# Kernel optimization log

Hardware: AMD Instinct MI355X
Metric: run time of the kernel (lower is better)

Reference implementation:

```python
import jax, jax.numpy as jnp
import numpy as np

N_NODES = 50000
N_EDGES = 800000
IN_DIM = 128
HID = 64
HEADS = 4
EDGE_DIM = 3
NEG_SLOPE = 0.2  # PyG GATv2 default


def setup_inputs() -> dict:
    key = jax.random.key(0)
    ks = jax.random.split(key, 16)
    def glorot(k, shape):
        fan_in = shape[0]
        return (jax.random.normal(k, shape, jnp.float32) / jnp.sqrt(jnp.float32(fan_in)))
    x = jax.random.normal(ks[0], (N_NODES, IN_DIM), jnp.float32)
    edge_attr = jax.random.normal(ks[1], (N_EDGES, EDGE_DIM), jnp.float32)
    edge_index = jax.random.randint(ks[2], (2, N_EDGES), 0, N_NODES, jnp.int32)
    # layer 1: GATv2Conv(IN_DIM -> HID, heads=HEADS, edge_dim=3, concat=True)
    W1l = glorot(ks[3], (IN_DIM, HEADS * HID))
    W1r = glorot(ks[4], (IN_DIM, HEADS * HID))
    W1e = glorot(ks[5], (EDGE_DIM, HEADS * HID))
    att1 = glorot(ks[6], (HEADS, HID))
    b1 = jnp.zeros((HEADS * HID,), jnp.float32)
    # layer 2: GATv2Conv(HEADS*HID -> 1, heads=1, edge_dim=3, concat=False)
    W2l = glorot(ks[7], (HEADS * HID, 1))
    W2r = glorot(ks[8], (HEADS * HID, 1))
    W2e = glorot(ks[9], (EDGE_DIM, 1))
    att2 = glorot(ks[10], (1, 1))
    b2 = jnp.zeros((1,), jnp.float32)
    return {"x": x, "edge_attr": edge_attr, "W1l": W1l, "W1r": W1r, "W1e": W1e,
            "att1": att1, "b1": b1, "W2l": W2l, "W2r": W2r, "W2e": W2e,
            "att2": att2, "b2": b2, "edge_index": edge_index}


def _add_self_loops(edge_index, edge_attr, n_nodes):
    # PyG GATv2Conv add_self_loops=True with fill_value='mean' for edge_attr
    loops = jnp.arange(n_nodes, dtype=edge_index.dtype)
    ei = jnp.concatenate([edge_index, jnp.stack([loops, loops])], axis=1)
    loop_attr = jnp.broadcast_to(edge_attr.mean(axis=0, keepdims=True),
                                 (n_nodes, edge_attr.shape[1]))
    ea = jnp.concatenate([edge_attr, loop_attr], axis=0)
    return ei, ea


def _gatv2(x, edge_index, edge_attr, Wl, Wr, We, att, bias, heads, concat):
    n = x.shape[0]
    c = Wl.shape[1] // heads
    src, dst = edge_index[0], edge_index[1]
    xl = (x @ Wl).reshape(n, heads, c)   # source-side transform
    xr = (x @ Wr).reshape(n, heads, c)   # target-side transform
    ef = (edge_attr @ We).reshape(-1, heads, c)
    m = jax.nn.leaky_relu(xl[src] + xr[dst] + ef, NEG_SLOPE)   # [E,H,C]
    logits = jnp.einsum('ehc,hc->eh', m, att)                  # [E,H]
    mx = jax.ops.segment_max(logits, dst, num_segments=n)      # segment softmax over dst
    a = jnp.exp(logits - mx[dst])
    denom = jax.ops.segment_sum(a, dst, num_segments=n)
    alpha = a / denom[dst]                                     # [E,H]
    out = jax.ops.segment_sum(xl[src] * alpha[:, :, None], dst, num_segments=n)  # [N,H,C]
    out = out.reshape(n, heads * c) if concat else out.mean(axis=1)
    return out + bias


def reference(x, edge_attr, W1l, W1r, W1e, att1, b1, W2l, W2r, W2e, att2, b2, edge_index):
    n = x.shape[0]
    ei, ea = _add_self_loops(edge_index, edge_attr, n)
    h = _gatv2(x, ei, ea, W1l, W1r, W1e, att1, b1, HEADS, True)
    h = jax.nn.elu(h)  # dropout identity in eval mode
    gat_scores = _gatv2(h, ei, ea, W2l, W2r, W2e, att2, b2, 1, False).squeeze(-1)
    portfolio_weights = jax.nn.softmax(gat_scores, axis=0)
    return portfolio_weights, gat_scores
```

## Files before the change

### kernel.cpp

```cpp
#include <hip/hip_runtime.h>
#include <hip/hip_bf16.h>
#include <hip/hip_fp16.h>

typedef __attribute__((ext_vector_type(8))) short short8;
typedef __attribute__((ext_vector_type(4))) float floatx4;
typedef __attribute__((ext_vector_type(4))) unsigned short ushortx4;
typedef _Float16 h2 __attribute__((ext_vector_type(2)));
typedef _Float16 h4 __attribute__((ext_vector_type(4)));
typedef _Float16 h8 __attribute__((ext_vector_type(8)));

#define N_NODESC 50000
#define MPAD     50016
#define N_EDGESC 800000
#define E_TOTC   850000
#define IN_DIMC  128
#define FDIM     256
#define HEADSC   4
#define HIDC     64
#define NEG_SLOPE 0.2f
#define RESCALE_THR 8.0f

#define SCAN_TILE 1024
#define SCAN_NB   ((N_NODESC + SCAN_TILE - 1) / SCAN_TILE)

__device__ __forceinline__ float wave_sum(float v){
  #pragma unroll
  for (int m = 32; m > 0; m >>= 1) v += __shfl_xor(v, m, 64);
  return v;
}
__device__ __forceinline__ float wave_max(float v){
  #pragma unroll
  for (int m = 32; m > 0; m >>= 1) v = fmaxf(v, __shfl_xor(v, m, 64));
  return v;
}

__device__ __forceinline__ h2 f2h2(float v){
  return __builtin_bit_cast(h2, __builtin_amdgcn_cvt_pkrtz(v, v));
}

__global__ __launch_bounds__(256) void k_mean(const float* __restrict__ ea,
                                              float* __restrict__ meanacc){
  float s0 = 0.f, s1 = 0.f, s2 = 0.f;
  for (int i = blockIdx.x * blockDim.x + threadIdx.x; i < N_EDGESC;
       i += gridDim.x * blockDim.x){
    s0 += ea[i*3+0]; s1 += ea[i*3+1]; s2 += ea[i*3+2];
  }
  s0 = wave_sum(s0); s1 = wave_sum(s1); s2 = wave_sum(s2);
  __shared__ float red[3][4];
  int lane = threadIdx.x & 63, w = threadIdx.x >> 6;
  if (lane == 0){ red[0][w] = s0; red[1][w] = s1; red[2][w] = s2; }
  __syncthreads();
  if (threadIdx.x == 0){
    float t0 = 0.f, t1 = 0.f, t2 = 0.f;
    for (int i = 0; i < 4; i++){ t0 += red[0][i]; t1 += red[1][i]; t2 += red[2][i]; }
    atomicAdd(&meanacc[0], t0); atomicAdd(&meanacc[1], t1); atomicAdd(&meanacc[2], t2);
  }
}

__global__ __launch_bounds__(256) void k_count(const int* __restrict__ ei,
                                               int* __restrict__ deg){
  int e = blockIdx.x * blockDim.x + threadIdx.x;
  if (e >= N_EDGESC) return;
  atomicAdd(&deg[ei[N_EDGESC + e]], 1);
}

__global__ __launch_bounds__(256) void k_cvtx(const float* __restrict__ x,
                                              _Float16* __restrict__ xb){
  size_t tid = (size_t)blockIdx.x * 256 + threadIdx.x;
  size_t base = tid * 4;
  const size_t NELEM = (size_t)N_NODESC * IN_DIMC;
  h4 o;
  if (base + 3 < NELEM){
    const float4* xp = (const float4*)(x + base);
    float4 v = *xp;
    o[0] = (_Float16)v.x; o[1] = (_Float16)v.y;
    o[2] = (_Float16)v.z; o[3] = (_Float16)v.w;
  } else {
    #pragma unroll
    for (int f = 0; f < 4; f++){
      size_t i = base + f;
      float v = (i < NELEM) ? x[i] : 0.f;
      o[f] = (_Float16)v;
    }
  }
  *(h4*)(xb + base) = o;
}

__global__ __launch_bounds__(256) void k_cvtw(const float* __restrict__ W1l,
                                              const float* __restrict__ W1r,
                                              _Float16* __restrict__ Bfrag){
  int idx = blockIdx.x * 256 + threadIdx.x;
  int mat = idx >> 15;
  int r   = idx & 32767;
  int k   = r >> 8, n = r & 255;
  float v = mat ? W1r[r] : W1l[r];
  int pos = (mat << 15) + (((k >> 3) << 8) + n) * 8 + (k & 7);
  Bfrag[pos] = (_Float16)v;
}

__global__ __launch_bounds__(256) void k_gemm_mfma(const _Float16* __restrict__ xb,
                                                   const _Float16* __restrict__ Bfrag,
                                                   _Float16* __restrict__ xl,
                                                   _Float16* __restrict__ xr){
  const int mat = blockIdx.y;
  const int r0  = blockIdx.x * 32;
  const int w = threadIdx.x >> 6, lane = threadIdx.x & 63;
  const int quad = lane >> 4, l16 = lane & 15;
  const _Float16* Bm = Bfrag + ((size_t)mat << 15);
  _Float16* C = mat ? xr : xl;

  h8 afr[2][4];
  #pragma unroll
  for (int ms = 0; ms < 2; ms++)
    #pragma unroll
    for (int ks = 0; ks < 4; ks++){
      const _Float16* p = xb + (size_t)(r0 + ms*16 + l16) * IN_DIMC + ks*32 + quad*8;
      afr[ms][ks] = *reinterpret_cast<const h8*>(p);
    }
  const int n0 = w * 64;
  floatx4 acc[2][4];
  #pragma unroll
  for (int ms = 0; ms < 2; ms++)
    #pragma unroll
    for (int ns = 0; ns < 4; ns++){
      floatx4 z = {0.f, 0.f, 0.f, 0.f};
      acc[ms][ns] = z;
    }
  #pragma unroll
  for (int ks = 0; ks < 4; ks++){
    #pragma unroll
    for (int ns = 0; ns < 4; ns++){
      int n = n0 + ns*16 + l16;
      int kblk = ks*4 + quad;
      h8 bfr = *reinterpret_cast<const h8*>(Bm + ((size_t)kblk*256 + n)*8);
      acc[0][ns] = __builtin_amdgcn_mfma_f32_16x16x32_f16(afr[0][ks], bfr, acc[0][ns], 0, 0, 0);
      acc[1][ns] = __builtin_amdgcn_mfma_f32_16x16x32_f16(afr[1][ks], bfr, acc[1][ns], 0, 0, 0);
    }
  }
  #pragma unroll
  for (int ms = 0; ms < 2; ms++)
    #pragma unroll
    for (int ns = 0; ns < 4; ns++){
      int col = n0 + ns*16 + l16;
      #pragma unroll
      for (int rg = 0; rg < 4; rg++){
        int row = r0 + ms*16 + quad*4 + rg;
        C[(size_t)row * FDIM + col] = (_Float16)acc[ms][ns][rg];
      }
    }
}

__global__ __launch_bounds__(256) void k_scan_pa(const int* __restrict__ deg,
                                                 int* __restrict__ pre,
                                                 int* __restrict__ bsum){
  int b = blockIdx.x, t = threadIdx.x;
  int lane = t & 63, w = t >> 6;
  int base = b * SCAN_TILE + t * 4;
  int4 v = {0, 0, 0, 0};
  if (base + 3 < N_NODESC){
    v = *(const int4*)(deg + base);
    v.x += 1; v.y += 1; v.z += 1; v.w += 1;
  } else {
    if (base + 0 < N_NODESC) v.x = deg[base + 0] + 1;
    if (base + 1 < N_NODESC) v.y = deg[base + 1] + 1;
    if (base + 2 < N_NODESC) v.z = deg[base + 2] + 1;
    if (base + 3 < N_NODESC) v.w = deg[base + 3] + 1;
  }
  int s = v.x + v.y + v.z + v.w;
  int inc = s;
  #pragma unroll
  for (int off = 1; off < 64; off <<= 1){
    int u = __shfl_up(inc, off, 64);
    if (lane >= off) inc += u;
  }
  __shared__ int wsum[4];
  if (lane == 63) wsum[w] = inc;
  __syncthreads();
  int wadd = 0;
  #pragma unroll
  for (int i = 0; i < 4; i++) if (i < w) wadd += wsum[i];
  int excl = inc - s + wadd;
  if (base + 3 < N_NODESC){
    int4 o;
    o.x = excl; o.y = o.x + v.x; o.z = o.y + v.y; o.w = o.z + v.z;
    *(int4*)(pre + base) = o;
  } else {
    int run = excl;
    if (base + 0 < N_NODESC){ pre[base + 0] = run; run += v.x; }
    if (base + 1 < N_NODESC){ pre[base + 1] = run; run += v.y; }
    if (base + 2 < N_NODESC){ pre[base + 2] = run; run += v.z; }
    if (base + 3 < N_NODESC){ pre[base + 3] = run; }
  }
  if (t == 255) bsum[b] = wsum[0] + wsum[1] + wsum[2] + wsum[3];
}

__global__ __launch_bounds__(64) void k_scan_pb(const int* __restrict__ bsum,
                                                int* __restrict__ boff,
                                                int* __restrict__ offsets){
  int lane = threadIdx.x;
  int s = (lane < SCAN_NB) ? bsum[lane] : 0;
  int inc = s;
  #pragma unroll
  for (int off = 1; off < 64; off <<= 1){
    int u = __shfl_up(inc, off, 64);
    if (lane >= off) inc += u;
  }
  if (lane < SCAN_NB) boff[lane] = inc - s;
  if (lane == 63) offsets[N_NODESC] = inc;
}

__global__ __launch_bounds__(256) void k_scan_pc(const int* __restrict__ pre,
                                                 const int* __restrict__ boff,
                                                 int* __restrict__ offsets,
                                                 int* __restrict__ cursor){
  int b = blockIdx.x;
  int base = b * SCAN_TILE + threadIdx.x * 4;
  int add = boff[b];
  if (base + 3 < N_NODESC){
    int4 p = *(const int4*)(pre + base);
    p.x += add; p.y += add; p.z += add; p.w += add;
    *(int4*)(offsets + base) = p;
    *(int4*)(cursor + base) = p;
  } else {
    #pragma unroll
    for (int f = 0; f < 4; f++){
      int i = base + f;
      if (i < N_NODESC){ int vv = pre[i] + add; offsets[i] = vv; cursor[i] = vv; }
    }
  }
}

__global__ __launch_bounds__(256) void k_scatter(const int* __restrict__ ei,
                                                 const float* __restrict__ ea,
                                                 const float* __restrict__ meanacc,
                                                 const int* __restrict__ offsets,
                                                 int* __restrict__ cursor,
                                                 float4* __restrict__ rec){
  int e = blockIdx.x * blockDim.x + threadIdx.x;
  if (e >= E_TOTC) return;
  int pos; float4 r;
  if (e < N_EDGESC){
    int src = ei[e], dst = ei[N_EDGESC + e];
    r.x = __int_as_float(src);
    r.y = ea[e*3+0]; r.z = ea[e*3+1]; r.w = ea[e*3+2];
    pos = atomicAdd(&cursor[dst], 1);
  } else {
    int i = e - N_EDGESC;
    const float inv = 1.0f / (float)N_EDGESC;
    r.x = __int_as_float(i);
    r.y = meanacc[0]*inv; r.z = meanacc[1]*inv; r.w = meanacc[2]*inv;
    pos = offsets[i + 1] - 1;
  }
  rec[pos] = r;
}

__global__ __launch_bounds__(256, 8) void k_attn1(const int* __restrict__ offsets,
                                                  const float4* __restrict__ rec,
                                                  const _Float16* __restrict__ xl,
                                                  const _Float16* __restrict__ xr,
                                                  const float* __restrict__ W1e,
                                                  const float* __restrict__ att1,
                                                  const float* __restrict__ b1,
                                                  const float* __restrict__ W2l,
                                                  const float* __restrict__ W2r,
                                                  float* __restrict__ sl,
                                                  float* __restrict__ sr){
  const int t = threadIdx.x, lane = t & 63, w = t >> 6;
  const int n = blockIdx.x * 4 + w;
  const int f0 = lane * 4;

  h2 xr01, xr23, w0a, w0b, w1a, w1b, w2a, w2b, at01, at23;
  {
    h4 xw = *(const h4*)(xr + (size_t)n * FDIM + f0);
    float4 a = *(const float4*)(W1e + f0);
    float4 b = *(const float4*)(W1e + FDIM + f0);
    float4 c = *(const float4*)(W1e + 2*FDIM + f0);
    float4 d = *(const float4*)(att1 + f0);
    xr01 = h2{xw[0], xw[1]};                  xr23 = h2{xw[2], xw[3]};
    w0a = h2{(_Float16)a.x, (_Float16)a.y};   w0b = h2{(_Float16)a.z, (_Float16)a.w};
    w1a = h2{(_Float16)b.x, (_Float16)b.y};   w1b = h2{(_Float16)b.z, (_Float16)b.w};
    w2a = h2{(_Float16)c.x, (_Float16)c.y};   w2b = h2{(_Float16)c.z, (_Float16)c.w};
    at01 = h2{(_Float16)d.x, (_Float16)d.y};  at23 = h2{(_Float16)d.z, (_Float16)d.w};
  }
  const h2 nsl2 = h2{(_Float16)NEG_SLOPE, (_Float16)NEG_SLOPE};
  const int beg = offsets[n], end = offsets[n + 1];
  const int last = end - 1;

  float m = -1e30f, den = 0.f;
  float acc0 = 0.f, acc1 = 0.f, acc2 = 0.f, acc3 = 0.f;

  float4 rc  = rec[beg];
  float4 rcn = rec[min(beg + 1, last)];
  int src0 = __builtin_amdgcn_readfirstlane(__float_as_int(rc.x));
  h4 raw = *(const h4*)(xl + (size_t)src0 * FDIM + f0);

  for (int j = beg; j < end; j++){
    const float e0 = rc.y, e1 = rc.z, e2 = rc.w;
    int srcn = __builtin_amdgcn_readfirstlane(__float_as_int(rcn.x));
    h4 rawn = *(const h4*)(xl + (size_t)srcn * FDIM + f0);
    rc = rcn;
    rcn = rec[min(j + 2, last)];

    h2 he0 = f2h2(e0);
    h2 he1 = f2h2(e1);
    h2 he2 = f2h2(e2);

    h2 x01 = h2{raw[0], raw[1]};
    h2 x23 = h2{raw[2], raw[3]};
    h2 v01 = x01 + xr01 + he0*w0a + he1*w1a + he2*w2a;
    h2 v23 = x23 + xr23 + he0*w0b + he1*w1b + he2*w2b;
    v01 = __builtin_elementwise_max(v01, nsl2 * v01);
    v23 = __builtin_elementwise_max(v23, nsl2 * v23);
    float pp = __builtin_amdgcn_fdot2(__builtin_bit_cast(__fp16 __attribute__((ext_vector_type(2))), v01),
                                      __builtin_bit_cast(__fp16 __attribute__((ext_vector_type(2))), at01),
                                      0.f, false);
    pp = __builtin_amdgcn_fdot2(__builtin_bit_cast(__fp16 __attribute__((ext_vector_type(2))), v23),
                                __builtin_bit_cast(__fp16 __attribute__((ext_vector_type(2))), at23),
                                pp, false);
    pp += __shfl_xor(pp, 1, 64);
    pp += __shfl_xor(pp, 2, 64);
    pp += __shfl_xor(pp, 4, 64);
    pp += __shfl_xor(pp, 8, 64);

    if (pp > m + RESCALE_THR){
      float corr = __expf(m - pp);
      den *= corr;
      acc0 *= corr; acc1 *= corr; acc2 *= corr; acc3 *= corr;
      m = pp;
    }
    float al = __expf(pp - m);
    den += al;
    acc0 = fmaf((float)raw[0], al, acc0);
    acc1 = fmaf((float)raw[1], al, acc1);
    acc2 = fmaf((float)raw[2], al, acc2);
    acc3 = fmaf((float)raw[3], al, acc3);

    raw = rawn;
  }

  float invd = 1.0f / den;
  float4 bb = *(const float4*)(b1 + f0);
  float h0 = acc0 * invd + bb.x;
  float h1 = acc1 * invd + bb.y;
  float h2v = acc2 * invd + bb.z;
  float h3 = acc3 * invd + bb.w;
  h0 = (h0 > 0.f) ? h0 : (__expf(h0) - 1.f);
  h1 = (h1 > 0.f) ? h1 : (__expf(h1) - 1.f);
  h2v = (h2v > 0.f) ? h2v : (__expf(h2v) - 1.f);
  h3 = (h3 > 0.f) ? h3 : (__expf(h3) - 1.f);
  float4 wl = *(const float4*)(W2l + f0);
  float4 wr = *(const float4*)(W2r + f0);
  float pa = h0*wl.x + h1*wl.y + h2v*wl.z + h3*wl.w;
  float pb = h0*wr.x + h1*wr.y + h2v*wr.z + h3*wr.w;
  pa = wave_sum(pa);
  pb = wave_sum(pb);
  if (lane == 0){ sl[n] = pa; sr[n] = pb; }
}

__device__ __forceinline__ unsigned fkey(float f){
  unsigned u = __float_as_uint(f);
  return u ^ ((u >> 31) ? 0xFFFFFFFFu : 0x80000000u);
}
__device__ __forceinline__ float funkey(unsigned k){
  unsigned u = (k >> 31) ? (k ^ 0x80000000u) : ~k;
  return __uint_as_float(u);
}

__global__ __launch_bounds__(256) void k_attn2(const int* __restrict__ offsets,
                                               const float4* __restrict__ rec,
                                               const float* __restrict__ W2e,
                                               const float* __restrict__ att2,
                                               const float* __restrict__ b2p,
                                               const float* __restrict__ sl,
                                               const float* __restrict__ sr,
                                               float* __restrict__ scores,
                                               float* __restrict__ out){
  int t = threadIdx.x, lane = t & 63;
  int n = blockIdx.x * 4 + (t >> 6);
  if (n >= N_NODESC) return;
  const float attv = att2[0];
  const float w2e0 = W2e[0], w2e1 = W2e[1], w2e2 = W2e[2];
  const float srn = sr[n];
  int beg = offsets[n], end = offsets[n + 1];
  float m = -1e30f, den = 0.f, num = 0.f;
  for (int j = beg + lane; j < end; j += 64){
    float4 rc = rec[j];
    float slv = sl[__float_as_int(rc.x)];
    float v = slv + srn + rc.y*w2e0 + rc.z*w2e1 + rc.w*w2e2;
    v = (v > 0.f) ? v : NEG_SLOPE * v;
    float lg = v * attv;
    float mn = fmaxf(m, lg);
    float corr = __expf(m - mn);
    float pe   = __expf(lg - mn);
    den = den * corr + pe;
    num = num * corr + pe * slv;
    m = mn;
  }
  float mg = wave_max(m);
  float scale = __expf(m - mg);
  float deng = wave_sum(den * scale);
  float numg = wave_sum(num * scale);
  if (lane == 0){
    float s = numg / deng + b2p[0];
    scores[n] = s;
    out[N_NODESC + n] = s;
  }
}

__global__ __launch_bounds__(256) void k_smax_max(const float* __restrict__ scores,
                                                  unsigned* __restrict__ redmax){
  float m = -1e30f;
  for (int i = blockIdx.x * blockDim.x + threadIdx.x; i < N_NODESC;
       i += gridDim.x * blockDim.x)
    m = fmaxf(m, scores[i]);
  m = wave_max(m);
  __shared__ float ws_[4];
  int lane = threadIdx.x & 63, w = threadIdx.x >> 6;
  if (lane == 0) ws_[w] = m;
  __syncthreads();
  if (threadIdx.x == 0){
    for (int i = 1; i < 4; i++) m = fmaxf(m, ws_[i]);
    atomicMax(redmax, fkey(m));
  }
}

__global__ __launch_bounds__(256) void k_smax_sum(const float* __restrict__ scores,
                                                  const unsigned* __restrict__ redmax,
                                                  float* __restrict__ redsum){
  float mx = funkey(*redmax);
  float s = 0.f;
  for (int i = blockIdx.x * blockDim.x + threadIdx.x; i < N_NODESC;
       i += gridDim.x * blockDim.x)
    s += __expf(scores[i] - mx);
  s = wave_sum(s);
  __shared__ float ws_[4];
  int lane = threadIdx.x & 63, w = threadIdx.x >> 6;
  if (lane == 0) ws_[w] = s;
  __syncthreads();
  if (threadIdx.x == 0){
    float t = 0.f;
    for (int i = 0; i < 4; i++) t += ws_[i];
    atomicAdd(redsum, t);
  }
}

__global__ __launch_bounds__(256) void k_smax_write(const float* __restrict__ scores,
                                                    const unsigned* __restrict__ redmax,
                                                    const float* __restrict__ redsum,
                                                    float* __restrict__ out){
  int i = blockIdx.x * blockDim.x + threadIdx.x;
  if (i >= N_NODESC) return;
  float mx = funkey(*redmax);
  float inv = 1.0f / (*redsum);
  out[i] = __expf(scores[i] - mx) * inv;
}

extern "C" void kernel_launch(void* const* d_in, const int* in_sizes, int n_in,
                              void* d_out, int out_size, void* d_ws, size_t ws_size,
                              hipStream_t stream) {
  const float* x    = (const float*)d_in[0];
  const float* ea   = (const float*)d_in[1];
  const float* W1l  = (const float*)d_in[2];
  const float* W1r  = (const float*)d_in[3];
  const float* W1e  = (const float*)d_in[4];
  const float* att1 = (const float*)d_in[5];
  const float* b1   = (const float*)d_in[6];
  const float* W2l  = (const float*)d_in[7];
  const float* W2r  = (const float*)d_in[8];
  const float* W2e  = (const float*)d_in[9];
  const float* att2 = (const float*)d_in[10];
  const float* b2   = (const float*)d_in[11];
  const int*   ei   = (const int*)d_in[12];
  float* out = (float*)d_out;

  char* w = (char*)d_ws;
  size_t off = 0;
  auto alloc = [&](size_t bytes) -> char* {
    char* p = w + off;
    off = (off + bytes + 255) & ~(size_t)255;
    return p;
  };
  float*    meanacc = (float*)alloc(16);
  unsigned* redmax  = (unsigned*)alloc(8);
  float*    redsum  = (float*)((char*)redmax + 4);
  int*      deg     = (int*)alloc((size_t)N_NODESC * 4);
  size_t zero_bytes = off;
  int*   offsets = (int*)alloc((size_t)(N_NODESC + 1) * 4);
  int*   cursor  = (int*)alloc((size_t)N_NODESC * 4);
  int*   pre     = (int*)alloc((size_t)N_NODESC * 4);
  int*   bsum    = (int*)alloc((size_t)SCAN_NB * 4);
  int*   boff    = (int*)alloc((size_t)SCAN_NB * 4);
  float4* rec    = (float4*)alloc((size_t)E_TOTC * 16);
  float* sl      = (float*)alloc((size_t)N_NODESC * 4);
  float* sr      = (float*)alloc((size_t)N_NODESC * 4);
  float* scores  = (float*)alloc((size_t)N_NODESC * 4);
  _Float16* xb    = (_Float16*)alloc((size_t)MPAD * IN_DIMC * 2);
  _Float16* Bfrag = (_Float16*)alloc((size_t)2 * 128 * 256 * 2);
  _Float16* xl    = (_Float16*)alloc((size_t)MPAD * FDIM * 2);
  _Float16* xr    = (_Float16*)alloc((size_t)MPAD * FDIM * 2);
  (void)ws_size; (void)in_sizes; (void)n_in; (void)out_size;

  hipMemsetAsync(d_ws, 0, zero_bytes, stream);

  k_mean  <<<400, 256, 0, stream>>>(ea, meanacc);
  k_count <<<(N_EDGESC + 255) / 256, 256, 0, stream>>>(ei, deg);
  k_cvtx  <<<(int)(((size_t)MPAD * IN_DIMC / 4 + 255) / 256), 256, 0, stream>>>(x, xb);
  k_cvtw  <<<256, 256, 0, stream>>>(W1l, W1r, Bfrag);
  k_scan_pa<<<SCAN_NB, 256, 0, stream>>>(deg, pre, bsum);
  k_scan_pb<<<1, 64, 0, stream>>>(bsum, boff, offsets);
  k_scan_pc<<<SCAN_NB, 256, 0, stream>>>(pre, boff, offsets, cursor);
  k_scatter<<<(E_TOTC + 255) / 256, 256, 0, stream>>>(ei, ea, meanacc, offsets,
                                                      cursor, rec);
  {
    dim3 g(MPAD / 32, 2);
    k_gemm_mfma<<<g, 256, 0, stream>>>(xb, Bfrag, xl, xr);
  }
  k_attn1 <<<N_NODESC / 4, 256, 0, stream>>>(offsets, rec, xl, xr,
                                             W1e, att1, b1, W2l, W2r, sl, sr);
  k_attn2 <<<(N_NODESC + 3) / 4, 256, 0, stream>>>(offsets, rec, W2e, att2, b2,
                                                   sl, sr, scores, out);
  k_smax_max <<<256, 256, 0, stream>>>(scores, redmax);
  k_smax_sum <<<256, 256, 0, stream>>>(scores, redmax, redsum);
  k_smax_write<<<(N_NODESC + 255) / 256, 256, 0, stream>>>(scores, redmax, redsum, out);
}
```

Measured before the change: 358.5 us.

## Split attn1 wave into two half-waves over edges, shrink attn2 groups to 16 lanes

In the layer-1 attention kernel each wave now handles two edges at once: each 32-lane half-wave processes alternate edges with 8 features per lane using 16-byte gathers. The two halves keep separate online-softmax states and merge them at the end with cross-half shuffles. This halves the serial edge loop length and widens each gather, at the cost of more registers and a merge step. The layer-2 kernel now uses 16 lanes per node instead of 64, which cuts idle lanes given an average degree of about 17.

Result: no change. 354.5 us (-1.1%).

```diff
diff --git a/kernel.cpp b/kernel.cpp
--- a/kernel.cpp
+++ b/kernel.cpp
@@ -4,10 +4,10 @@
 
 typedef __attribute__((ext_vector_type(8))) short short8;
 typedef __attribute__((ext_vector_type(4))) float floatx4;
-typedef __attribute__((ext_vector_type(4))) unsigned short ushortx4;
 typedef _Float16 h2 __attribute__((ext_vector_type(2)));
 typedef _Float16 h4 __attribute__((ext_vector_type(4)));
 typedef _Float16 h8 __attribute__((ext_vector_type(8)));
+typedef __fp16 fp16x2 __attribute__((ext_vector_type(2)));
 
 #define N_NODESC 50000
 #define MPAD     50016
@@ -33,9 +33,23 @@
   for (int m = 32; m > 0; m >>= 1) v = fmaxf(v, __shfl_xor(v, m, 64));
   return v;
 }
+__device__ __forceinline__ float g16_sum(float v){
+  #pragma unroll
+  for (int m = 8; m > 0; m >>= 1) v += __shfl_xor(v, m, 64);
+  return v;
+}
+__device__ __forceinline__ float g16_max(float v){
+  #pragma unroll
+  for (int m = 8; m > 0; m >>= 1) v = fmaxf(v, __shfl_xor(v, m, 64));
+  return v;
+}
 
 __device__ __forceinline__ h2 f2h2(float v){
   return __builtin_bit_cast(h2, __builtin_amdgcn_cvt_pkrtz(v, v));
+}
+__device__ __forceinline__ float fdot2(h2 a, h2 b, float c){
+  return __builtin_amdgcn_fdot2(__builtin_bit_cast(fp16x2, a),
+                                __builtin_bit_cast(fp16x2, b), c, false);
 }
 
 __global__ __launch_bounds__(256) void k_mean(const float* __restrict__ ea,
@@ -267,93 +281,112 @@
                                                   float* __restrict__ sr){
   const int t = threadIdx.x, lane = t & 63, w = t >> 6;
   const int n = blockIdx.x * 4 + w;
-  const int f0 = lane * 4;
-
-  h2 xr01, xr23, w0a, w0b, w1a, w1b, w2a, w2b, at01, at23;
+  const int half = lane >> 5, l32 = lane & 31;
+  const int f0 = l32 * 8;
+
+  h2 xrp[4], w0p[4], w1p[4], w2p[4], atp[4];
   {
-    h4 xw = *(const h4*)(xr + (size_t)n * FDIM + f0);
-    float4 a = *(const float4*)(W1e + f0);
-    float4 b = *(const float4*)(W1e + FDIM + f0);
-    float4 c = *(const float4*)(W1e + 2*FDIM + f0);
-    float4 d = *(const float4*)(att1 + f0);
-    xr01 = h2{xw[0], xw[1]};                  xr23 = h2{xw[2], xw[3]};
-    w0a = h2{(_Float16)a.x, (_Float16)a.y};   w0b = h2{(_Float16)a.z, (_Float16)a.w};
-    w1a = h2{(_Float16)b.x, (_Float16)b.y};   w1b = h2{(_Float16)b.z, (_Float16)b.w};
-    w2a = h2{(_Float16)c.x, (_Float16)c.y};   w2b = h2{(_Float16)c.z, (_Float16)c.w};
-    at01 = h2{(_Float16)d.x, (_Float16)d.y};  at23 = h2{(_Float16)d.z, (_Float16)d.w};
+    h8 xw = *(const h8*)(xr + (size_t)n * FDIM + f0);
+    #pragma unroll
+    for (int k = 0; k < 4; k++) xrp[k] = h2{xw[2*k], xw[2*k+1]};
+    float4 a0 = *(const float4*)(W1e + f0);
+    float4 a1 = *(const float4*)(W1e + f0 + 4);
+    w0p[0]=h2{(_Float16)a0.x,(_Float16)a0.y}; w0p[1]=h2{(_Float16)a0.z,(_Float16)a0.w};
+    w0p[2]=h2{(_Float16)a1.x,(_Float16)a1.y}; w0p[3]=h2{(_Float16)a1.z,(_Float16)a1.w};
+    float4 b0 = *(const float4*)(W1e + FDIM + f0);
+    float4 b4 = *(const float4*)(W1e + FDIM + f0 + 4);
+    w1p[0]=h2{(_Float16)b0.x,(_Float16)b0.y}; w1p[1]=h2{(_Float16)b0.z,(_Float16)b0.w};
+    w1p[2]=h2{(_Float16)b4.x,(_Float16)b4.y}; w1p[3]=h2{(_Float16)b4.z,(_Float16)b4.w};
+    float4 c0 = *(const float4*)(W1e + 2*FDIM + f0);
+    float4 c4 = *(const float4*)(W1e + 2*FDIM + f0 + 4);
+    w2p[0]=h2{(_Float16)c0.x,(_Float16)c0.y}; w2p[1]=h2{(_Float16)c0.z,(_Float16)c0.w};
+    w2p[2]=h2{(_Float16)c4.x,(_Float16)c4.y}; w2p[3]=h2{(_Float16)c4.z,(_Float16)c4.w};
+    float4 d0 = *(const float4*)(att1 + f0);
+    float4 d4 = *(const float4*)(att1 + f0 + 4);
+    atp[0]=h2{(_Float16)d0.x,(_Float16)d0.y}; atp[1]=h2{(_Float16)d0.z,(_Float16)d0.w};
+    atp[2]=h2{(_Float16)d4.x,(_Float16)d4.y}; atp[3]=h2{(_Float16)d4.z,(_Float16)d4.w};
   }
   const h2 nsl2 = h2{(_Float16)NEG_SLOPE, (_Float16)NEG_SLOPE};
   const int beg = offsets[n], end = offsets[n + 1];
   const int last = end - 1;
 
   float m = -1e30f, den = 0.f;
-  float acc0 = 0.f, acc1 = 0.f, acc2 = 0.f, acc3 = 0.f;
-
-  float4 rc  = rec[beg];
-  float4 rcn = rec[min(beg + 1, last)];
-  int src0 = __builtin_amdgcn_readfirstlane(__float_as_int(rc.x));
-  h4 raw = *(const h4*)(xl + (size_t)src0 * FDIM + f0);
-
-  for (int j = beg; j < end; j++){
+  float acc[8] = {0.f,0.f,0.f,0.f,0.f,0.f,0.f,0.f};
+
+  int j = beg + half;
+  float4 rc  = rec[min(j, last)];
+  float4 rcn = rec[min(j + 2, last)];
+  unsigned off0 = ((unsigned)__float_as_int(rc.x) << 8) + f0;
+  h8 raw = *(const h8*)(xl + off0);
+
+  for (; j < end; j += 2){
+    unsigned offn = ((unsigned)__float_as_int(rcn.x) << 8) + f0;
+    h8 rawn = *(const h8*)(xl + offn);
     const float e0 = rc.y, e1 = rc.z, e2 = rc.w;
-    int srcn = __builtin_amdgcn_readfirstlane(__float_as_int(rcn.x));
-    h4 rawn = *(const h4*)(xl + (size_t)srcn * FDIM + f0);
     rc = rcn;
-    rcn = rec[min(j + 2, last)];
-
-    h2 he0 = f2h2(e0);
-    h2 he1 = f2h2(e1);
-    h2 he2 = f2h2(e2);
-
-    h2 x01 = h2{raw[0], raw[1]};
-    h2 x23 = h2{raw[2], raw[3]};
-    h2 v01 = x01 + xr01 + he0*w0a + he1*w1a + he2*w2a;
-    h2 v23 = x23 + xr23 + he0*w0b + he1*w1b + he2*w2b;
-    v01 = __builtin_elementwise_max(v01, nsl2 * v01);
-    v23 = __builtin_elementwise_max(v23, nsl2 * v23);
-    float pp = __builtin_amdgcn_fdot2(__builtin_bit_cast(__fp16 __attribute__((ext_vector_type(2))), v01),
-                                      __builtin_bit_cast(__fp16 __attribute__((ext_vector_type(2))), at01),
-                                      0.f, false);
-    pp = __builtin_amdgcn_fdot2(__builtin_bit_cast(__fp16 __attribute__((ext_vector_type(2))), v23),
-                                __builtin_bit_cast(__fp16 __attribute__((ext_vector_type(2))), at23),
-                                pp, false);
+    rcn = rec[min(j + 4, last)];
+
+    h2 he0 = f2h2(e0), he1 = f2h2(e1), he2 = f2h2(e2);
+    float pp = 0.f;
+    #pragma unroll
+    for (int k = 0; k < 4; k++){
+      h2 xk = h2{raw[2*k], raw[2*k+1]};
+      h2 v = xk + xrp[k] + he0*w0p[k] + he1*w1p[k] + he2*w2p[k];
+      v = __builtin_elementwise_max(v, nsl2 * v);
+      pp = fdot2(v, atp[k], pp);
+    }
     pp += __shfl_xor(pp, 1, 64);
     pp += __shfl_xor(pp, 2, 64);
     pp += __shfl_xor(pp, 4, 64);
-    pp += __shfl_xor(pp, 8, 64);
 
     if (pp > m + RESCALE_THR){
       float corr = __expf(m - pp);
       den *= corr;
-      acc0 *= corr; acc1 *= corr; acc2 *= corr; acc3 *= corr;
+      #pragma unroll
+      for (int k = 0; k < 8; k++) acc[k] *= corr;
       m = pp;
     }
     float al = __expf(pp - m);
     den += al;
-    acc0 = fmaf((float)raw[0], al, acc0);
-    acc1 = fmaf((float)raw[1], al, acc1);
-    acc2 = fmaf((float)raw[2], al, acc2);
-    acc3 = fmaf((float)raw[3], al, acc3);
+    #pragma unroll
+    for (int k = 0; k < 8; k++) acc[k] = fmaf((float)raw[k], al, acc[k]);
 
     raw = rawn;
   }
 
-  float invd = 1.0f / den;
-  float4 bb = *(const float4*)(b1 + f0);
-  float h0 = acc0 * invd + bb.x;
-  float h1 = acc1 * invd + bb.y;
-  float h2v = acc2 * invd + bb.z;
-  float h3 = acc3 * invd + bb.w;
-  h0 = (h0 > 0.f) ? h0 : (__expf(h0) - 1.f);
-  h1 = (h1 > 0.f) ? h1 : (__expf(h1) - 1.f);
-  h2v = (h2v > 0.f) ? h2v : (__expf(h2v) - 1.f);
-  h3 = (h3 > 0.f) ? h3 : (__expf(h3) - 1.f);
-  float4 wl = *(const float4*)(W2l + f0);
-  float4 wr = *(const float4*)(W2r + f0);
-  float pa = h0*wl.x + h1*wl.y + h2v*wl.z + h3*wl.w;
-  float pb = h0*wr.x + h1*wr.y + h2v*wr.z + h3*wr.w;
-  pa = wave_sum(pa);
-  pb = wave_sum(pb);
+  float m_o   = __shfl_xor(m, 32, 64);
+  float den_o = __shfl_xor(den, 32, 64);
+  float m_t = fmaxf(m, m_o);
+  float sc   = __expf(m - m_t);
+  float sc_o = __expf(m_o - m_t);
+  float den_t = den * sc + den_o * sc_o;
+  float invd = 1.0f / den_t;
+
+  float4 bb0 = *(const float4*)(b1 + f0);
+  float4 bb4 = *(const float4*)(b1 + f0 + 4);
+  float bb[8] = {bb0.x,bb0.y,bb0.z,bb0.w,bb4.x,bb4.y,bb4.z,bb4.w};
+  float hv[8];
+  #pragma unroll
+  for (int k = 0; k < 8; k++){
+    float a_o = __shfl_xor(acc[k], 32, 64);
+    float tot = acc[k] * sc + a_o * sc_o;
+    float h = tot * invd + bb[k];
+    hv[k] = (h > 0.f) ? h : (__expf(h) - 1.f);
+  }
+  float4 l0 = *(const float4*)(W2l + f0);
+  float4 l4 = *(const float4*)(W2l + f0 + 4);
+  float4 r0 = *(const float4*)(W2r + f0);
+  float4 r4 = *(const float4*)(W2r + f0 + 4);
+  float wl[8] = {l0.x,l0.y,l0.z,l0.w,l4.x,l4.y,l4.z,l4.w};
+  float wr[8] = {r0.x,r0.y,r0.z,r0.w,r4.x,r4.y,r4.z,r4.w};
+  float pa = 0.f, pb = 0.f;
+  #pragma unroll
+  for (int k = 0; k < 8; k++){ pa += hv[k]*wl[k]; pb += hv[k]*wr[k]; }
+  #pragma unroll
+  for (int msk = 16; msk > 0; msk >>= 1){
+    pa += __shfl_xor(pa, msk, 64);
+    pb += __shfl_xor(pb, msk, 64);
+  }
   if (lane == 0){ sl[n] = pa; sr[n] = pb; }
 }
 
@@ -375,15 +408,15 @@
                                                const float* __restrict__ sr,
                                                float* __restrict__ scores,
                                                float* __restrict__ out){
-  int t = threadIdx.x, lane = t & 63;
-  int n = blockIdx.x * 4 + (t >> 6);
+  int t = threadIdx.x, l16 = t & 15;
+  int n = blockIdx.x * 16 + (t >> 4);
   if (n >= N_NODESC) return;
   const float attv = att2[0];
   const float w2e0 = W2e[0], w2e1 = W2e[1], w2e2 = W2e[2];
   const float srn = sr[n];
   int beg = offsets[n], end = offsets[n + 1];
   float m = -1e30f, den = 0.f, num = 0.f;
-  for (int j = beg + lane; j < end; j += 64){
+  for (int j = beg + l16; j < end; j += 16){
     float4 rc = rec[j];
     float slv = sl[__float_as_int(rc.x)];
     float v = slv + srn + rc.y*w2e0 + rc.z*w2e1 + rc.w*w2e2;
@@ -396,11 +429,11 @@
     num = num * corr + pe * slv;
     m = mn;
   }
-  float mg = wave_max(m);
+  float mg = g16_max(m);
   float scale = __expf(m - mg);
-  float deng = wave_sum(den * scale);
-  float numg = wave_sum(num * scale);
-  if (lane == 0){
+  float deng = g16_sum(den * scale);
+  float numg = g16_sum(num * scale);
+  if (l16 == 0){
     float s = numg / deng + b2p[0];
     scores[n] = s;
     out[N_NODESC + n] = s;
@@ -517,8 +550,8 @@
   }
   k_attn1 <<<N_NODESC / 4, 256, 0, stream>>>(offsets, rec, xl, xr,
                                              W1e, att1, b1, W2l, W2r, sl, sr);
-  k_attn2 <<<(N_NODESC + 3) / 4, 256, 0, stream>>>(offsets, rec, W2e, att2, b2,
-                                                   sl, sr, scores, out);
+  k_attn2 <<<(N_NODESC + 15) / 16, 256, 0, stream>>>(offsets, rec, W2e, att2, b2,
+                                                     sl, sr, scores, out);
   k_smax_max <<<256, 256, 0, stream>>>(scores, redmax);
   k_smax_sum <<<256, 256, 0, stream>>>(scores, redmax, redsum);
   k_smax_write<<<(N_NODESC + 255) / 256, 256, 0, stream>>>(scores, redmax, redsum, out);
```
